# Performance work log

Hardware: AMD Instinct MI355X
Metric: run time of the kernel (lower is better)

Reference implementation:

```python
import jax, jax.numpy as jnp
import numpy as np

N_NODES = 100000
N_EDGES = 600000
N_FEAT = 128
DIM = 128
N_LAYERS = 4
N_GRAPHS = 1000
BN_EPS = 1e-4


def setup_inputs() -> dict:
    key = jax.random.key(0)
    ks = jax.random.split(key, 12)
    s = 0.05
    x = jax.random.normal(ks[0], (N_NODES, N_FEAT), dtype=jnp.float32)
    edge_index = jax.random.randint(ks[1], (2, N_EDGES), 0, N_NODES, dtype=jnp.int64)
    batch = jnp.sort(jax.random.randint(ks[2], (N_NODES,), 0, N_GRAPHS, dtype=jnp.int64))
    pre_w = jax.random.normal(ks[3], (N_FEAT, DIM), dtype=jnp.float32) * s
    pre_b = jnp.zeros((DIM,), dtype=jnp.float32)
    # GIN MLP weights (first layer input is DIM since pre projects to DIM)
    conv_w1 = jax.random.normal(ks[4], (N_LAYERS, DIM, DIM), dtype=jnp.float32) * s
    conv_w2 = jax.random.normal(ks[5], (N_LAYERS, DIM, DIM), dtype=jnp.float32) * s
    bn_g = jnp.ones((N_LAYERS, DIM), dtype=jnp.float32)
    bn_b = jnp.zeros((N_LAYERS, DIM), dtype=jnp.float32)
    ed = DIM * N_LAYERS  # embedding_dim = 512
    ff_w1 = jax.random.normal(ks[6], (ed, ed), dtype=jnp.float32) * s
    ff_w2 = jax.random.normal(ks[7], (ed, ed), dtype=jnp.float32) * s
    ff_w3 = jax.random.normal(ks[8], (ed, ed), dtype=jnp.float32) * s
    ff_sc = jax.random.normal(ks[9], (ed, ed), dtype=jnp.float32) * s
    return dict(x=x, edge_index=edge_index, batch=batch, pre_w=pre_w, pre_b=pre_b,
                conv_w1=conv_w1, conv_w2=conv_w2, bn_g=bn_g, bn_b=bn_b,
                ff_w1=ff_w1, ff_w2=ff_w2, ff_w3=ff_w3, ff_sc=ff_sc)


def reference(x, edge_index, batch, pre_w, pre_b, conv_w1, conv_w2, bn_g, bn_b,
              ff_w1, ff_w2, ff_w3, ff_sc):
    lrelu = jax.nn.leaky_relu  # negative_slope=0.01 matches torch default
    n = x.shape[0]
    src, dst = edge_index[0], edge_index[1]

    h = x @ pre_w + pre_b  # [N, DIM]
    xs = []
    for i in range(conv_w1.shape[0]):
        # GINConv (eps=0): nn(x + sum_{j->i} x_j); gather at src, scatter-add at dst
        agg = jax.ops.segment_sum(h[src], dst, num_segments=n)
        h2 = h + agg
        h2 = lrelu(h2 @ conv_w1[i]) @ conv_w2[i]
        # BatchNorm1d (training mode, biased variance, eps=1e-4)
        mean = jnp.mean(h2, axis=0)
        var = jnp.var(h2, axis=0)
        h = (h2 - mean) * jax.lax.rsqrt(var + BN_EPS) * bn_g[i] + bn_b[i]
        xs.append(h)

    # global_add_pool per layer, then concat -> [G, DIM*L]
    pooled = [jax.ops.segment_sum(hl, batch, num_segments=N_GRAPHS) for hl in xs]
    y = jnp.concatenate(pooled, axis=1)

    z = lrelu(lrelu(lrelu(y @ ff_w1) @ ff_w2) @ ff_w3) + y @ ff_sc
    return z
```

## Files before the change

kernel.cpp:

```cpp
#include <hip/hip_runtime.h>
#include <hip/hip_bf16.h>

typedef __hip_bfloat16 bf16;
typedef unsigned int u32;
typedef __attribute__((ext_vector_type(8))) short short8v;
typedef __attribute__((ext_vector_type(4))) float f32x4;

__device__ __forceinline__ float lrelu_f(float v) { return v > 0.f ? v : 0.01f * v; }
__device__ __forceinline__ float bf_lo(u32 u) { return __uint_as_float(u << 16); }
__device__ __forceinline__ float bf_hi(u32 u) { return __uint_as_float(u & 0xffff0000u); }
__device__ __forceinline__ unsigned short bbits(float v) {
    union { bf16 b; unsigned short s; } u; u.b = __float2bfloat16(v); return u.s;
}
__device__ __forceinline__ u32 pack2(float a, float b) {
    return (u32)bbits(a) | ((u32)bbits(b) << 16);
}
__device__ __forceinline__ float ld_ext(const void* p, size_t idx, int f32f) {
    return f32f ? ((const float*)p)[idx] : __bfloat162float(((const bf16*)p)[idx]);
}

__global__ void probe_k(const int* __restrict__ ei, const int* __restrict__ batch,
                        const u32* __restrict__ bng, int nedges, int nnodes,
                        int* __restrict__ flags, float* __restrict__ scaleA,
                        float* __restrict__ shiftA)
{
    __shared__ int nz[2];
    if (threadIdx.x < 2) nz[threadIdx.x] = 0;
    __syncthreads();
    int t = threadIdx.x;
    if (ei[(nedges + 2 * t) | 1] != 0) atomicAdd(&nz[0], 1);
    if (batch[((nnodes >> 1) + 2 * t) | 1] != 0) atomicAdd(&nz[1], 1);
    if (t < 128) { scaleA[t] = 1.f; shiftA[t] = 0.f; }
    __syncthreads();
    if (t == 0) {
        flags[0] = (nz[0] == 0) ? 1 : 0;
        flags[1] = (nz[1] == 0) ? 1 : 0;
        flags[2] = (bng[0] == 0x3F800000u) ? 1 : 0;
    }
}

__global__ __launch_bounds__(256)
void hist_k(const int* __restrict__ ei, int* __restrict__ deg, int nedges,
            const int* __restrict__ flags)
{
    int e = blockIdx.x * 256 + threadIdx.x;
    if (e >= nedges) return;
    int f = flags[0];
    int dst = f ? ei[(nedges + e) << 1] : ei[nedges + e];
    atomicAdd(&deg[dst], 1);
}

__global__ __launch_bounds__(256)
void scan1_k(const int* __restrict__ deg, int* __restrict__ bsum, int n)
{
    __shared__ int l[256];
    int t = threadIdx.x, i = blockIdx.x * 256 + t;
    l[t] = (i < n) ? deg[i] : 0;
    __syncthreads();
    for (int off = 128; off > 0; off >>= 1) {
        if (t < off) l[t] += l[t + off];
        __syncthreads();
    }
    if (t == 0) bsum[blockIdx.x] = l[0];
}
__global__ __launch_bounds__(1024)
void scan2_k(int* __restrict__ bsum, int nb)
{
    __shared__ int l[1024];
    int t = threadIdx.x;
    int orig = (t < nb) ? bsum[t] : 0;
    l[t] = orig;
    __syncthreads();
    for (int off = 1; off < 1024; off <<= 1) {
        int v = (t >= off) ? l[t - off] : 0;
        __syncthreads();
        l[t] += v;
        __syncthreads();
    }
    if (t < nb) bsum[t] = l[t] - orig;
}
__global__ __launch_bounds__(256)
void scan3_k(const int* __restrict__ deg, const int* __restrict__ bsum,
             int* __restrict__ rowptr, int* __restrict__ cursor, int n)
{
    __shared__ int l[256];
    int t = threadIdx.x, i = blockIdx.x * 256 + t;
    int d = (i < n) ? deg[i] : 0;
    l[t] = d;
    __syncthreads();
    for (int off = 1; off < 256; off <<= 1) {
        int v = (t >= off) ? l[t - off] : 0;
        __syncthreads();
        l[t] += v;
        __syncthreads();
    }
    int excl = l[t] - d + bsum[blockIdx.x];
    if (i < n) {
        rowptr[i] = excl;
        cursor[i] = excl;
        if (i == n - 1) rowptr[n] = excl + d;
    }
}

__global__ __launch_bounds__(256)
void fill_k(const int* __restrict__ ei, int* __restrict__ cursor,
            int* __restrict__ srcs, int nedges, const int* __restrict__ flags)
{
    int e = blockIdx.x * 256 + threadIdx.x;
    if (e >= nedges) return;
    int f = flags[0];
    int src = ei[e << f];
    int dst = f ? ei[(nedges + e) << 1] : ei[nedges + e];
    int pos = atomicAdd(&cursor[dst], 1);
    srcs[pos] = src;
}

__global__ __launch_bounds__(256)
void wprep_all_k(const void* __restrict__ pre_w, const void* __restrict__ w1,
                 const void* __restrict__ w2, const void* __restrict__ f0,
                 const void* __restrict__ f1, const void* __restrict__ f2,
                 const void* __restrict__ f3, bf16* __restrict__ Wf,
                 const int* __restrict__ flags)
{
    int e = blockIdx.x * 256 + threadIdx.x;
    if (e >= 1196032) return;
    const void* W; int K, wstride, l, r;
    if (e < 16384)       { W = pre_w; K = 128; wstride = 128; l = 0; r = e; }
    else if (e < 81920)  { int q = e - 16384; W = w1; K = 128; wstride = 128; l = q >> 14; r = q & 16383; }
    else if (e < 147456) { int q = e - 81920; W = w2; K = 128; wstride = 128; l = q >> 14; r = q & 16383; }
    else {
        int q = e - 147456; int m = q >> 18; r = q & 262143;
        W = (m == 0) ? f0 : (m == 1) ? f1 : (m == 2) ? f2 : f3;
        K = 512; wstride = 512; l = 0;
    }
    int KS = K >> 5;
    int j = r & 7, lane = (r >> 3) & 63;
    int rem = r >> 9;
    int ks = rem % KS, nt = rem / KS;
    int k = ks * 32 + ((lane >> 4) << 3) + j;
    int n = nt * 16 + (lane & 15);
    Wf[e] = __float2bfloat16(ld_ext(W, (size_t)(l * K + k) * wstride + n, flags[2]));
}

template<int SRC, int MODE, int OBF>
__global__ __launch_bounds__(256)
void mgemm_k(const void* __restrict__ A, const bf16* __restrict__ Wf,
             const void* __restrict__ bias, void* __restrict__ out,
             int nrows, int K, int astride, int ostride, const int* __restrict__ flags)
{
    const int KS = K >> 5;
    const int t = threadIdx.x, w = t >> 6, lane = t & 63;
    const int quad = lane >> 4, lr = lane & 15;
    const int rbase = blockIdx.x * 64 + w * 16;
    const int arow = min(rbase + lr, nrows - 1);
    const int ntg0 = blockIdx.y * 8;
    const int f32f = flags[2];

    f32x4 acc[8];
    #pragma unroll
    for (int i = 0; i < 8; ++i) acc[i] = (f32x4){0.f, 0.f, 0.f, 0.f};

    for (int ks = 0; ks < KS; ++ks) {
        const int kof = ks * 32 + quad * 8;
        short8v a;
        if (SRC == 0 || f32f) {
            const float* Af = (const float*)A + (size_t)arow * astride + kof;
            float4 p0 = *(const float4*)Af;
            float4 p1 = *(const float4*)(Af + 4);
            a[0] = (short)bbits(p0.x); a[1] = (short)bbits(p0.y);
            a[2] = (short)bbits(p0.z); a[3] = (short)bbits(p0.w);
            a[4] = (short)bbits(p1.x); a[5] = (short)bbits(p1.y);
            a[6] = (short)bbits(p1.z); a[7] = (short)bbits(p1.w);
        } else {
            a = *(const short8v*)((const short*)A + (size_t)arow * astride + kof);
        }
        #pragma unroll
        for (int nt = 0; nt < 8; ++nt) {
            const short8v b = *(const short8v*)&Wf[(((size_t)(ntg0 + nt) * KS + ks) * 64 + lane) * 8];
            acc[nt] = __builtin_amdgcn_mfma_f32_16x16x32_bf16(a, b, acc[nt], 0, 0, 0);
        }
    }

    #pragma unroll
    for (int nt = 0; nt < 8; ++nt) {
        const int col = (ntg0 + nt) * 16 + lr;
        float bv = 0.f;
        if (MODE == 0 && bias != nullptr) bv = ld_ext(bias, col, f32f);
        #pragma unroll
        for (int r = 0; r < 4; ++r) {
            int orow = rbase + quad * 4 + r;
            if (orow < nrows) {
                float v = acc[nt][r] + bv;
                if (MODE == 1) v = lrelu_f(v);
                if (OBF) ((bf16*)out)[(size_t)orow * ostride + col] = __float2bfloat16(v);
                else     ((float*)out)[(size_t)orow * ostride + col] = v;
            }
        }
    }
}

__global__ __launch_bounds__(256, 4)
void conv_k(const u32* __restrict__ aggb, const bf16* __restrict__ Wf1,
            const bf16* __restrict__ Wf2, u32* __restrict__ h2,
            float* __restrict__ psum, float* __restrict__ psq, int nrows)
{
    __shared__ bf16 tls[4][32][136];
    __shared__ float lsum[128], lsq[128];
    const int t = threadIdx.x, w = t >> 6, lane = t & 63;
    const int quad = lane >> 4, lr = lane & 15;
    const int rbase = blockIdx.x * 128 + w * 32;
    const int arow0 = min(rbase + lr, nrows - 1);
    const int arow1 = min(rbase + 16 + lr, nrows - 1);
    if (t < 128) { lsum[t] = 0.f; lsq[t] = 0.f; }

    f32x4 acc[2][8];
    #pragma unroll
    for (int h = 0; h < 2; ++h)
        #pragma unroll
        for (int i = 0; i < 8; ++i) acc[h][i] = (f32x4){0.f, 0.f, 0.f, 0.f};

    #pragma unroll
    for (int ks = 0; ks < 4; ++ks) {
        short8v a0 = *(const short8v*)&aggb[(size_t)arow0 * 64 + ks * 16 + quad * 4];
        short8v a1 = *(const short8v*)&aggb[(size_t)arow1 * 64 + ks * 16 + quad * 4];
        #pragma unroll
        for (int nt = 0; nt < 8; ++nt) {
            const short8v b = *(const short8v*)&Wf1[((nt * 4 + ks) * 64 + lane) * 8];
            acc[0][nt] = __builtin_amdgcn_mfma_f32_16x16x32_bf16(a0, b, acc[0][nt], 0, 0, 0);
            acc[1][nt] = __builtin_amdgcn_mfma_f32_16x16x32_bf16(a1, b, acc[1][nt], 0, 0, 0);
        }
    }
    #pragma unroll
    for (int h = 0; h < 2; ++h)
        #pragma unroll
        for (int nt = 0; nt < 8; ++nt)
            #pragma unroll
            for (int r = 0; r < 4; ++r)
                tls[w][h * 16 + quad * 4 + r][nt * 16 + lr] = __float2bfloat16(lrelu_f(acc[h][nt][r]));
    __syncthreads();

    f32x4 acc2[2][8];
    #pragma unroll
    for (int h = 0; h < 2; ++h)
        #pragma unroll
        for (int i = 0; i < 8; ++i) acc2[h][i] = (f32x4){0.f, 0.f, 0.f, 0.f};
    #pragma unroll
    for (int ks = 0; ks < 4; ++ks) {
        short8v a0 = *(const short8v*)&tls[w][lr][ks * 32 + quad * 8];
        short8v a1 = *(const short8v*)&tls[w][16 + lr][ks * 32 + quad * 8];
        #pragma unroll
        for (int nt = 0; nt < 8; ++nt) {
            const short8v b = *(const short8v*)&Wf2[((nt * 4 + ks) * 64 + lane) * 8];
            acc2[0][nt] = __builtin_amdgcn_mfma_f32_16x16x32_bf16(a0, b, acc2[0][nt], 0, 0, 0);
            acc2[1][nt] = __builtin_amdgcn_mfma_f32_16x16x32_bf16(a1, b, acc2[1][nt], 0, 0, 0);
        }
    }
    #pragma unroll
    for (int h = 0; h < 2; ++h)
        #pragma unroll
        for (int nt = 0; nt < 8; ++nt) {
            float s = 0.f, q = 0.f;
            #pragma unroll
            for (int r = 0; r < 4; ++r) {
                int orow = rbase + h * 16 + quad * 4 + r;
                if (orow < nrows) {
                    float v = acc2[h][nt][r];
                    s += v; q += v * v;
                    ((bf16*)h2)[(size_t)orow * 128 + nt * 16 + lr] = __float2bfloat16(v);
                }
            }
            atomicAdd(&lsum[nt * 16 + lr], s);
            atomicAdd(&lsq[nt * 16 + lr], q);
        }
    __syncthreads();
    if (t < 128) {
        psum[(size_t)blockIdx.x * 128 + t] = lsum[t];
        psq[(size_t)blockIdx.x * 128 + t] = lsq[t];
    }
}

__global__ __launch_bounds__(256)
void reduce_bn_k(const float* __restrict__ psum, const float* __restrict__ psq,
                 const void* __restrict__ g, const void* __restrict__ b,
                 float* __restrict__ scale, float* __restrict__ shift,
                 float inv_n, int layer, int nblk, const int* __restrict__ flags)
{
    __shared__ float ls[256], lq[256];
    int c = blockIdx.x, t = threadIdx.x;
    float s = 0.f, q = 0.f;
    for (int i = t; i < nblk; i += 256) {
        s += psum[(size_t)i * 128 + c];
        q += psq[(size_t)i * 128 + c];
    }
    ls[t] = s; lq[t] = q;
    __syncthreads();
    for (int off = 128; off > 0; off >>= 1) {
        if (t < off) { ls[t] += ls[t + off]; lq[t] += lq[t + off]; }
        __syncthreads();
    }
    if (t == 0) {
        int f32f = flags[2];
        size_t off = (size_t)layer * 128 + c;
        float mean = ls[0] * inv_n;
        float var = lq[0] * inv_n - mean * mean;
        float sc = ld_ext(g, off, f32f) * rsqrtf(fmaxf(var, 0.f) + 1e-4f);
        scale[c] = sc;
        shift[c] = ld_ext(b, off, f32f) - mean * sc;
    }
}

__global__ __launch_bounds__(256)
void aggregate_k(const int* __restrict__ rowptr, const int* __restrict__ srcs,
                 const u32* __restrict__ h2, u32* __restrict__ aggb,
                 const float* __restrict__ scale, const float* __restrict__ shift, int nnodes)
{
    int node = blockIdx.x * 4 + (threadIdx.x >> 6);
    if (node >= nnodes) return;
    int lane = threadIdx.x & 63;
    u32 u = h2[(size_t)node * 64 + lane];
    float ax = bf_lo(u), ay = bf_hi(u);
    int lo = rowptr[node], hi = rowptr[node + 1];
    int e = lo;
    for (; e + 4 <= hi; e += 4) {
        int s0 = srcs[e], s1 = srcs[e + 1], s2 = srcs[e + 2], s3 = srcs[e + 3];
        u32 v0 = h2[(size_t)s0 * 64 + lane];
        u32 v1 = h2[(size_t)s1 * 64 + lane];
        u32 v2 = h2[(size_t)s2 * 64 + lane];
        u32 v3 = h2[(size_t)s3 * 64 + lane];
        ax += bf_lo(v0) + bf_lo(v1) + bf_lo(v2) + bf_lo(v3);
        ay += bf_hi(v0) + bf_hi(v1) + bf_hi(v2) + bf_hi(v3);
    }
    for (; e < hi; ++e) {
        u32 v = h2[(size_t)srcs[e] * 64 + lane];
        ax += bf_lo(v);
        ay += bf_hi(v);
    }
    float cnt = (float)(hi - lo + 1);
    int c = lane * 2;
    float r0 = fmaf(ax, scale[c], shift[c] * cnt);
    float r1 = fmaf(ay, scale[c + 1], shift[c + 1] * cnt);
    aggb[(size_t)node * 64 + lane] = pack2(r0, r1);
}

__device__ __forceinline__ int lower_bound_b(const int* b, int n, int key, int fb)
{
    int lo = 0, hi = n;
    while (lo < hi) {
        int m = (lo + hi) >> 1;
        if (b[m << fb] < key) lo = m + 1; else hi = m;
    }
    return lo;
}

__global__ __launch_bounds__(256)
void pool_k(const u32* __restrict__ h2, const int* __restrict__ batch,
            float* __restrict__ y, int layer, int nnodes, int ngraphs,
            const float* __restrict__ scale, const float* __restrict__ shift,
            const int* __restrict__ flags)
{
    int g = blockIdx.x * 4 + (threadIdx.x >> 6);
    if (g >= ngraphs) return;
    int t = threadIdx.x & 63;
    int fb = flags[1];
    int lo = lower_bound_b(batch, nnodes, g, fb);
    int hi = lower_bound_b(batch, nnodes, g + 1, fb);
    float s0 = 0.f, s1 = 0.f;
    int i = lo;
    for (; i + 4 <= hi; i += 4) {
        u32 u0 = h2[(size_t)i * 64 + t];
        u32 u1 = h2[(size_t)(i + 1) * 64 + t];
        u32 u2 = h2[(size_t)(i + 2) * 64 + t];
        u32 u3 = h2[(size_t)(i + 3) * 64 + t];
        s0 += bf_lo(u0) + bf_lo(u1) + bf_lo(u2) + bf_lo(u3);
        s1 += bf_hi(u0) + bf_hi(u1) + bf_hi(u2) + bf_hi(u3);
    }
    for (; i < hi; ++i) {
        u32 u = h2[(size_t)i * 64 + t];
        s0 += bf_lo(u);
        s1 += bf_hi(u);
    }
    float cnt = (float)(hi - lo);
    int c = t * 2;
    float* yp = &y[(size_t)g * 512 + layer * 128 + c];
    yp[0] = fmaf(s0, scale[c], shift[c] * cnt);
    yp[1] = fmaf(s1, scale[c + 1], shift[c + 1] * cnt);
}

__global__ __launch_bounds__(256)
void final_k(const float* __restrict__ a, const float* __restrict__ b,
             float* __restrict__ out, int n)
{
    int i = blockIdx.x * 256 + threadIdx.x;
    if (i < n) out[i] = a[i] + b[i];
}

extern "C" void kernel_launch(void* const* d_in, const int* in_sizes, int n_in,
                              void* d_out, int out_size, void* d_ws, size_t ws_size,
                              hipStream_t stream)
{
    const void* x       = d_in[0];
    const int*  ei      = (const int*)d_in[1];
    const int*  batch   = (const int*)d_in[2];
    const void* pre_w   = d_in[3];
    const void* pre_b   = d_in[4];
    const void* conv_w1 = d_in[5];
    const void* conv_w2 = d_in[6];
    const void* bn_g    = d_in[7];
    const void* bn_b    = d_in[8];

    const int n_nodes  = in_sizes[2];
    const int n_edges  = in_sizes[1] / 2;
    const int n_graphs = out_size / 512;
    const size_t nf = (size_t)n_nodes * 128;
    const int nsb = (n_nodes + 255) / 256;
    const int nblk = (n_nodes + 127) / 128;

    float* ws      = (float*)d_ws;
    int*   flags   = (int*)ws;
    int*   bsum    = (int*)(ws + 16);
    float* scaleA  = ws + 1056;
    float* shiftA  = scaleA + 5 * 128;
    float* psum    = shiftA + 5 * 128;
    float* psq     = psum + (size_t)nblk * 128;
    float* y       = psq + (size_t)nblk * 128;
    float* tA      = y  + (size_t)n_graphs * 512;
    float* tB      = tA + (size_t)n_graphs * 512;
    u32*   bufA    = (u32*)(tB + (size_t)n_graphs * 512);
    u32*   bufB    = bufA + nf / 2;
    int*   deg     = (int*)(bufB + nf / 2);
    int*   rowptr  = deg + n_nodes;
    int*   srcs    = rowptr + n_nodes + 1;
    bf16*  Wfn     = (bf16*)(((uintptr_t)(srcs + n_edges) + 15) & ~(uintptr_t)15);
    bf16*  Wff     = Wfn + 9 * 16384;

    probe_k<<<1, 256, 0, stream>>>(ei, batch, (const u32*)bn_g, n_edges, n_nodes,
                                   flags, scaleA, shiftA);

    hipMemsetAsync(deg, 0, n_nodes * sizeof(int), stream);
    hist_k<<<(n_edges + 255) / 256, 256, 0, stream>>>(ei, deg, n_edges, flags);
    scan1_k<<<nsb, 256, 0, stream>>>(deg, bsum, n_nodes);
    scan2_k<<<1, 1024, 0, stream>>>(bsum, nsb);
    scan3_k<<<nsb, 256, 0, stream>>>(deg, bsum, rowptr, deg, n_nodes);
    fill_k<<<(n_edges + 255) / 256, 256, 0, stream>>>(ei, deg, srcs, n_edges, flags);

    wprep_all_k<<<(1196032 + 255) / 256, 256, 0, stream>>>(
        pre_w, conv_w1, conv_w2, d_in[9], d_in[10], d_in[11], d_in[12], Wfn, flags);

    const dim3 gpre((n_nodes + 63) / 64, 1);
    const dim3 gconv(nblk, 1);
    const dim3 gf((n_graphs + 63) / 64, 4);

    mgemm_k<1, 0, 1><<<gpre, 256, 0, stream>>>(x, Wfn, pre_b, bufA, n_nodes, 128, 128, 128, flags);

    for (int l = 0; l < 4; ++l) {
        const u32* src = (l & 1) ? bufB : bufA;
        u32*       dst = (l & 1) ? bufA : bufB;
        aggregate_k<<<(n_nodes + 3) / 4, 256, 0, stream>>>(
            rowptr, srcs, src, dst, scaleA + l * 128, shiftA + l * 128, n_nodes);
        conv_k<<<gconv, 256, 0, stream>>>(dst, Wfn + (1 + l) * 16384, Wfn + (5 + l) * 16384,
                                          dst , psum, psq, n_nodes);
        reduce_bn_k<<<128, 256, 0, stream>>>(psum, psq, bn_g, bn_b,
                                             scaleA + (l + 1) * 128, shiftA + (l + 1) * 128,
                                             1.f / (float)n_nodes, l, nblk, flags);
        pool_k<<<(n_graphs + 3) / 4, 256, 0, stream>>>(
            dst, batch, y, l, n_nodes, n_graphs,
            scaleA + (l + 1) * 128, shiftA + (l + 1) * 128, flags);
    }

    mgemm_k<0, 0, 0><<<gf, 256, 0, stream>>>(y,  Wff + 3ull * 262144, nullptr, tB, n_graphs, 512, 512, 512, flags);
    mgemm_k<0, 1, 0><<<gf, 256, 0, stream>>>(y,  Wff + 0ull * 262144, nullptr, tA, n_graphs, 512, 512, 512, flags);
    mgemm_k<0, 1, 0><<<gf, 256, 0, stream>>>(tA, Wff + 1ull * 262144, nullptr, y,  n_graphs, 512, 512, 512, flags);
    mgemm_k<0, 1, 0><<<gf, 256, 0, stream>>>(y,  Wff + 2ull * 262144, nullptr, tA, n_graphs, 512, 512, 512, flags);

    final_k<<<(n_graphs * 512 + 255) / 256, 256, 0, stream>>>(tA, tB, (float*)d_out, n_graphs * 512);
}
```

Measured before the change: 856.1 us.

## Make conv kernel persistent with register-resident weights and transposed MFMA

Turns the GIN MLP kernel into a persistent grid of 512 blocks. Each wave holds its half of both weight matrices in registers, and the block loops over 16-node tiles, computing W^T·x so the weights serve as the A operand. BN partial sums are accumulated in registers and flushed to shared memory once per block, so reduce_bn works on 512 partials instead of about 782. The aim is to stop reloading weights from global memory for every tile. The cost is higher register use (occupancy lowered to 2), two block-wide barriers per tile, and a fixed bufA/bufB ping-pong in which h2 is written to bufA.

```diff
diff --git a/kernel.cpp b/kernel.cpp
--- a/kernel.cpp
+++ b/kernel.cpp
@@ -199,83 +199,101 @@
     }
 }
 
-__global__ __launch_bounds__(256, 4)
+__global__ __launch_bounds__(256, 2)
 void conv_k(const u32* __restrict__ aggb, const bf16* __restrict__ Wf1,
             const bf16* __restrict__ Wf2, u32* __restrict__ h2,
-            float* __restrict__ psum, float* __restrict__ psq, int nrows)
-{
-    __shared__ bf16 tls[4][32][136];
-    __shared__ float lsum[128], lsq[128];
+            float* __restrict__ psum, float* __restrict__ psq,
+            int nrows, int ntiles, int npairs)
+{
+    __shared__ bf16 PT[2][16][136];
+    __shared__ float sblk[128], qblk[128];
     const int t = threadIdx.x, w = t >> 6, lane = t & 63;
     const int quad = lane >> 4, lr = lane & 15;
-    const int rbase = blockIdx.x * 128 + w * 32;
-    const int arow0 = min(rbase + lr, nrows - 1);
-    const int arow1 = min(rbase + 16 + lr, nrows - 1);
-    if (t < 128) { lsum[t] = 0.f; lsq[t] = 0.f; }
-
-    f32x4 acc[2][8];
+    const int pair = w >> 1, hw = w & 1;
+    const int gpair = blockIdx.x * 2 + pair;
+    const int chb = hw * 64;
+
+    short8v w1f[4][4], w2f[4][4];
     #pragma unroll
-    for (int h = 0; h < 2; ++h)
+    for (int i = 0; i < 4; ++i)
         #pragma unroll
-        for (int i = 0; i < 8; ++i) acc[h][i] = (f32x4){0.f, 0.f, 0.f, 0.f};
-
+        for (int ks = 0; ks < 4; ++ks) {
+            int ntb = hw * 4 + i;
+            w1f[i][ks] = *(const short8v*)&Wf1[((ntb * 4 + ks) * 64 + lane) * 8];
+            w2f[i][ks] = *(const short8v*)&Wf2[((ntb * 4 + ks) * 64 + lane) * 8];
+        }
+
+    if (t < 128) { sblk[t] = 0.f; qblk[t] = 0.f; }
+    __syncthreads();
+
+    f32x4 s8[4], q8[4];
     #pragma unroll
-    for (int ks = 0; ks < 4; ++ks) {
-        short8v a0 = *(const short8v*)&aggb[(size_t)arow0 * 64 + ks * 16 + quad * 4];
-        short8v a1 = *(const short8v*)&aggb[(size_t)arow1 * 64 + ks * 16 + quad * 4];
-        #pragma unroll
-        for (int nt = 0; nt < 8; ++nt) {
-            const short8v b = *(const short8v*)&Wf1[((nt * 4 + ks) * 64 + lane) * 8];
-            acc[0][nt] = __builtin_amdgcn_mfma_f32_16x16x32_bf16(a0, b, acc[0][nt], 0, 0, 0);
-            acc[1][nt] = __builtin_amdgcn_mfma_f32_16x16x32_bf16(a1, b, acc[1][nt], 0, 0, 0);
-        }
-    }
-    #pragma unroll
-    for (int h = 0; h < 2; ++h)
-        #pragma unroll
-        for (int nt = 0; nt < 8; ++nt)
+    for (int i = 0; i < 4; ++i) { s8[i] = (f32x4){0,0,0,0}; q8[i] = (f32x4){0,0,0,0}; }
+
+    const int iters = (ntiles + npairs - 1) / npairs;
+    for (int it = 0; it < iters; ++it) {
+        const int tile = gpair + it * npairs;
+        const bool act = tile < ntiles;
+        const int nodeu = act ? tile * 16 + lr : 0;
+        const int node = min(nodeu, nrows - 1);
+        const bool valid = act && (nodeu < nrows);
+
+        if (act) {
+            f32x4 acc[4];
             #pragma unroll
-            for (int r = 0; r < 4; ++r)
-                tls[w][h * 16 + quad * 4 + r][nt * 16 + lr] = __float2bfloat16(lrelu_f(acc[h][nt][r]));
-    __syncthreads();
-
-    f32x4 acc2[2][8];
-    #pragma unroll
-    for (int h = 0; h < 2; ++h)
-        #pragma unroll
-        for (int i = 0; i < 8; ++i) acc2[h][i] = (f32x4){0.f, 0.f, 0.f, 0.f};
-    #pragma unroll
-    for (int ks = 0; ks < 4; ++ks) {
-        short8v a0 = *(const short8v*)&tls[w][lr][ks * 32 + quad * 8];
-        short8v a1 = *(const short8v*)&tls[w][16 + lr][ks * 32 + quad * 8];
-        #pragma unroll
-        for (int nt = 0; nt < 8; ++nt) {
-            const short8v b = *(const short8v*)&Wf2[((nt * 4 + ks) * 64 + lane) * 8];
-            acc2[0][nt] = __builtin_amdgcn_mfma_f32_16x16x32_bf16(a0, b, acc2[0][nt], 0, 0, 0);
-            acc2[1][nt] = __builtin_amdgcn_mfma_f32_16x16x32_bf16(a1, b, acc2[1][nt], 0, 0, 0);
-        }
-    }
-    #pragma unroll
-    for (int h = 0; h < 2; ++h)
-        #pragma unroll
-        for (int nt = 0; nt < 8; ++nt) {
-            float s = 0.f, q = 0.f;
+            for (int i = 0; i < 4; ++i) acc[i] = (f32x4){0,0,0,0};
             #pragma unroll
-            for (int r = 0; r < 4; ++r) {
-                int orow = rbase + h * 16 + quad * 4 + r;
-                if (orow < nrows) {
-                    float v = acc2[h][nt][r];
-                    s += v; q += v * v;
-                    ((bf16*)h2)[(size_t)orow * 128 + nt * 16 + lr] = __float2bfloat16(v);
+            for (int ks = 0; ks < 4; ++ks) {
+                const short8v bfrag = *(const short8v*)&aggb[(size_t)node * 64 + ks * 16 + quad * 4];
+                #pragma unroll
+                for (int i = 0; i < 4; ++i)
+                    acc[i] = __builtin_amdgcn_mfma_f32_16x16x32_bf16(w1f[i][ks], bfrag, acc[i], 0, 0, 0);
+            }
+            #pragma unroll
+            for (int i = 0; i < 4; ++i) {
+                u32* dp = (u32*)&PT[pair][lr][chb + i * 16 + quad * 4];
+                dp[0] = pack2(lrelu_f(acc[i][0]), lrelu_f(acc[i][1]));
+                dp[1] = pack2(lrelu_f(acc[i][2]), lrelu_f(acc[i][3]));
+            }
+        }
+        __syncthreads();
+        if (act) {
+            f32x4 acc2[4];
+            #pragma unroll
+            for (int i = 0; i < 4; ++i) acc2[i] = (f32x4){0,0,0,0};
+            #pragma unroll
+            for (int ks = 0; ks < 4; ++ks) {
+                const short8v pfrag = *(const short8v*)&PT[pair][lr][ks * 32 + quad * 8];
+                #pragma unroll
+                for (int i = 0; i < 4; ++i)
+                    acc2[i] = __builtin_amdgcn_mfma_f32_16x16x32_bf16(w2f[i][ks], pfrag, acc2[i], 0, 0, 0);
+            }
+            if (valid) {
+                #pragma unroll
+                for (int i = 0; i < 4; ++i) {
+                    u32* o = &h2[(size_t)nodeu * 64 + (chb >> 1) + i * 8 + quad * 2];
+                    o[0] = pack2(acc2[i][0], acc2[i][1]);
+                    o[1] = pack2(acc2[i][2], acc2[i][3]);
+                    s8[i] += acc2[i];
+                    q8[i] += acc2[i] * acc2[i];
                 }
             }
-            atomicAdd(&lsum[nt * 16 + lr], s);
-            atomicAdd(&lsq[nt * 16 + lr], q);
+        }
+        __syncthreads();
+    }
+
+    #pragma unroll
+    for (int i = 0; i < 4; ++i)
+        #pragma unroll
+        for (int r = 0; r < 4; ++r) {
+            int ch = chb + i * 16 + quad * 4 + r;
+            atomicAdd(&sblk[ch], s8[i][r]);
+            atomicAdd(&qblk[ch], q8[i][r]);
         }
     __syncthreads();
     if (t < 128) {
-        psum[(size_t)blockIdx.x * 128 + t] = lsum[t];
-        psq[(size_t)blockIdx.x * 128 + t] = lsq[t];
+        psum[(size_t)blockIdx.x * 128 + t] = sblk[t];
+        psq[(size_t)blockIdx.x * 128 + t] = qblk[t];
     }
 }
 
@@ -413,7 +431,9 @@
     const int n_graphs = out_size / 512;
     const size_t nf = (size_t)n_nodes * 128;
     const int nsb = (n_nodes + 255) / 256;
-    const int nblk = (n_nodes + 127) / 128;
+    const int NCONVB = 512;
+    const int ntiles = (n_nodes + 15) / 16;
+    const int npairs = NCONVB * 2;
 
     float* ws      = (float*)d_ws;
     int*   flags   = (int*)ws;
@@ -421,8 +441,8 @@
     float* scaleA  = ws + 1056;
     float* shiftA  = scaleA + 5 * 128;
     float* psum    = shiftA + 5 * 128;
-    float* psq     = psum + (size_t)nblk * 128;
-    float* y       = psq + (size_t)nblk * 128;
+    float* psq     = psum + (size_t)NCONVB * 128;
+    float* y       = psq + (size_t)NCONVB * 128;
     float* tA      = y  + (size_t)n_graphs * 512;
     float* tB      = tA + (size_t)n_graphs * 512;
     u32*   bufA    = (u32*)(tB + (size_t)n_graphs * 512);
@@ -447,23 +467,20 @@
         pre_w, conv_w1, conv_w2, d_in[9], d_in[10], d_in[11], d_in[12], Wfn, flags);
 
     const dim3 gpre((n_nodes + 63) / 64, 1);
-    const dim3 gconv(nblk, 1);
     const dim3 gf((n_graphs + 63) / 64, 4);
 
     mgemm_k<1, 0, 1><<<gpre, 256, 0, stream>>>(x, Wfn, pre_b, bufA, n_nodes, 128, 128, 128, flags);
 
     for (int l = 0; l < 4; ++l) {
-        const u32* src = (l & 1) ? bufB : bufA;
-        u32*       dst = (l & 1) ? bufA : bufB;
         aggregate_k<<<(n_nodes + 3) / 4, 256, 0, stream>>>(
-            rowptr, srcs, src, dst, scaleA + l * 128, shiftA + l * 128, n_nodes);
-        conv_k<<<gconv, 256, 0, stream>>>(dst, Wfn + (1 + l) * 16384, Wfn + (5 + l) * 16384,
-                                          dst , psum, psq, n_nodes);
+            rowptr, srcs, bufA, bufB, scaleA + l * 128, shiftA + l * 128, n_nodes);
+        conv_k<<<NCONVB, 256, 0, stream>>>(bufB, Wfn + (1 + l) * 16384, Wfn + (5 + l) * 16384,
+                                           bufA, psum, psq, n_nodes, ntiles, npairs);
         reduce_bn_k<<<128, 256, 0, stream>>>(psum, psq, bn_g, bn_b,
                                              scaleA + (l + 1) * 128, shiftA + (l + 1) * 128,
-                                             1.f / (float)n_nodes, l, nblk, flags);
+                                             1.f / (float)n_nodes, l, NCONVB, flags);
         pool_k<<<(n_graphs + 3) / 4, 256, 0, stream>>>(
-            dst, batch, y, l, n_nodes, n_graphs,
+            bufA, batch, y, l, n_nodes, n_graphs,
             scaleA + (l + 1) * 128, shiftA + (l + 1) * 128, flags);
     }
 
```

Result: faster. 811.3 us (-5.2%).
